# Kernel tuning notes

Hardware: AMD Instinct MI355X
Metric: run time of the kernel (lower is better)

## Reference

```python
import jax, jax.numpy as jnp
import numpy as np

B, L, D, P = 8, 2048, 1024, 256


def _ln(x):
    # LayerNorm without scale/offset (haiku default eps=1e-5)
    m = x.mean(-1, keepdims=True)
    v = x.var(-1, keepdims=True)
    return (x - m) * jax.lax.rsqrt(v + 1e-5)


def _s5(u, Lam_re, Lam_im, B_re, B_im, C_re, C_im, D_diag, log_step):
    # S5 diagonal SSM, ZOH discretization, parallel associative scan.
    Lam = Lam_re + 1j * Lam_im                      # (P,)
    dt = jnp.exp(log_step)                          # (P,)
    Lam_bar = jnp.exp(Lam * dt)                     # (P,)
    Bc = B_re + 1j * B_im                           # (P, D)
    B_bar = ((Lam_bar - 1.0) / Lam)[:, None] * Bc   # (P, D)
    Bu = jnp.einsum('bld,pd->blp', u.astype(B_bar.dtype), B_bar)  # (B, L, P)
    A = jnp.broadcast_to(Lam_bar, Bu.shape)

    def binop(e1, e2):
        a1, b1 = e1
        a2, b2 = e2
        return a1 * a2, a2 * b1 + b2

    _, xs = jax.lax.associative_scan(binop, (A, Bu), axis=1)  # (B, L, P)
    Cc = C_re + 1j * C_im                            # (D, P)
    return 2.0 * jnp.einsum('blp,dp->bld', xs, Cc).real + D_diag * u


def setup_inputs() -> dict:
    key = jax.random.key(0)
    ks = jax.random.split(key, 16)
    inp = {
        'y': jax.random.normal(ks[0], (B, L, D), jnp.float32),
        't': jax.random.normal(ks[1], (B, D), jnp.float32),
        # modulation projection m: Linear(D -> 6D)  (random instead of zero-init so output is non-trivial)
        'Wm': jax.random.normal(ks[2], (D, 6 * D), jnp.float32) * 0.02,
        'bm': jax.random.normal(ks[3], (6 * D,), jnp.float32) * 0.02,
        # S5Dual params
        'Lam_re': -0.5 * jnp.ones((P,), jnp.float32),
        'Lam_im': jnp.pi * jnp.arange(P, dtype=jnp.float32),
        'B_re': jax.random.normal(ks[4], (P, D), jnp.float32) / np.sqrt(D),
        'B_im': jax.random.normal(ks[5], (P, D), jnp.float32) / np.sqrt(D),
        'C_re': jax.random.normal(ks[6], (D, P), jnp.float32) / np.sqrt(P),
        'C_im': jax.random.normal(ks[7], (D, P), jnp.float32) / np.sqrt(P),
        'D_diag': jax.random.normal(ks[8], (D,), jnp.float32),
        'log_step': jax.random.uniform(ks[9], (P,), jnp.float32,
                                       np.log(0.001), np.log(0.1)),
        # AdaLN (norm2) projection: Linear(D -> 2D)
        'Wc': jax.random.normal(ks[10], (D, 2 * D), jnp.float32) * 0.02,
        'bc': jax.random.normal(ks[11], (2 * D,), jnp.float32) * 0.02,
        # FeedForward: pre Linear(D -> 4D), pos Linear(4D -> D) (random instead of zero-init)
        'W1': jax.random.normal(ks[12], (D, 4 * D), jnp.float32) / np.sqrt(D),
        'b1': jnp.zeros((4 * D,), jnp.float32),
        'W2': jax.random.normal(ks[13], (4 * D, D), jnp.float32) / np.sqrt(4 * D) * 0.1,
        'b2': jnp.zeros((D,), jnp.float32),
    }
    return inp


def reference(y, t, Wm, bm, Lam_re, Lam_im, B_re, B_im, C_re, C_im,
              D_diag, log_step, Wc, bc, W1, b1, W2, b2):
    # m(t) -> 6-way split
    mod = t @ Wm + bm
    shift_a, scale_a, gate_a, shift_ff, scale_ff, gate_ff = jnp.split(mod, 6, axis=-1)

    # S5 block with AdaLN-style modulation
    y_mod = _ln(y) * (1 + scale_a[:, None]) + shift_a[:, None]
    a_y = _s5(y_mod, Lam_re, Lam_im, B_re, B_im, C_re, C_im, D_diag, log_step)
    y = y + gate_a[:, None] * a_y

    # FFN block: norm2 is AdaLN(cond=t) composed with modulate(shift_ff, scale_ff)
    cond = t @ Wc + bc
    scale_c, shift_c = jnp.split(cond, 2, axis=-1)
    y_norm = _ln(y) * (1 + scale_c[:, None]) + shift_c[:, None]
    y_mod = y_norm * (1 + scale_ff[:, None]) + shift_ff[:, None]
    h = jax.nn.gelu(y_mod @ W1 + b1)
    ff_y = h @ W2 + b2
    return y + gate_ff[:, None] * ff_y
```

## Files before the change

### kernel.cpp

```cpp
#include <hip/hip_runtime.h>
#include <hip/hip_bf16.h>

#define Bsz 8
#define Lseq 2048
#define Dm 1024
#define Pst 256
#define BL (Bsz*Lseq)

typedef short bf16x8 __attribute__((ext_vector_type(8)));
typedef float f32x4  __attribute__((ext_vector_type(4)));

__device__ __forceinline__ float4 ldg4(const float* p){ return *reinterpret_cast<const float4*>(p); }
__device__ __forceinline__ ushort f2bf(float f){
    __hip_bfloat16 h = __float2bfloat16(f);
    return *reinterpret_cast<ushort*>(&h);
}
__device__ __forceinline__ float bf2f(ushort u){
    __hip_bfloat16 h = *reinterpret_cast<__hip_bfloat16*>(&u);
    return __bfloat162float(h);
}

__global__ __launch_bounds__(256) void proj_k(
    const float* __restrict__ T, const float* __restrict__ W,
    const float* __restrict__ bias, float* __restrict__ Out, int N)
{
    __shared__ float ts[Dm];
    int b = blockIdx.y;
    int j = blockIdx.x * 256 + threadIdx.x;
    for (int i = threadIdx.x; i < Dm; i += 256) ts[i] = T[b*Dm + i];
    __syncthreads();
    float s = bias[j];
    #pragma unroll 4
    for (int d = 0; d < Dm; ++d) s += ts[d] * W[(size_t)d*N + j];
    Out[(size_t)b*N + j] = s;
}

__global__ __launch_bounds__(256) void ssm_setup_k(
    const float* __restrict__ Lam_re, const float* __restrict__ Lam_im,
    const float* __restrict__ B_re, const float* __restrict__ B_im,
    const float* __restrict__ log_step, float* __restrict__ lam, ushort* __restrict__ Bbar_bf)
{
    int p = blockIdx.x;
    float lr = Lam_re[p], li = Lam_im[p];
    float dt = expf(log_step[p]);
    float e  = expf(lr*dt);
    float cr = e * cosf(li*dt);
    float ci = e * sinf(li*dt);
    float d2 = lr*lr + li*li;
    float nr = cr - 1.0f, ni = ci;
    float gr = (nr*lr + ni*li) / d2;
    float gi = (ni*lr - nr*li) / d2;
    if (threadIdx.x == 0) { lam[2*p] = cr; lam[2*p+1] = ci; }
    for (int d = threadIdx.x; d < Dm; d += 256) {
        float br = B_re[(size_t)p*Dm + d], bi = B_im[(size_t)p*Dm + d];
        Bbar_bf[(size_t)p*Dm + d]         = f2bf(gr*br - gi*bi);
        Bbar_bf[(size_t)(Pst+p)*Dm + d]   = f2bf(gr*bi + gi*br);
    }
}

__global__ __launch_bounds__(256) void ccat_k(
    const float* __restrict__ C_re, const float* __restrict__ C_im, ushort* __restrict__ Ccat_bf)
{
    int d = blockIdx.x;
    int p = threadIdx.x;
    Ccat_bf[(size_t)d*(2*Pst) + p]       = f2bf( 2.0f*C_re[(size_t)d*Pst + p]);
    Ccat_bf[(size_t)d*(2*Pst) + Pst + p] = f2bf(-2.0f*C_im[(size_t)d*Pst + p]);
}

__global__ __launch_bounds__(256) void transp_k(
    const float* __restrict__ in, ushort* __restrict__ out, int R, int C)
{
    __shared__ float tile[32][33];
    int tx = threadIdx.x & 31, ty = threadIdx.x >> 5;
    int r0 = blockIdx.y*32, c0 = blockIdx.x*32;
    #pragma unroll
    for (int j = 0; j < 4; ++j)
        tile[ty + j*8][tx] = in[(size_t)(r0 + ty + j*8)*C + c0 + tx];
    __syncthreads();
    #pragma unroll
    for (int j = 0; j < 4; ++j)
        out[(size_t)(c0 + ty + j*8)*R + r0 + tx] = f2bf(tile[tx][ty + j*8]);
}

template<int MODE>
__global__ __launch_bounds__(256) void ln_mod_k(
    const float* __restrict__ X, ushort* __restrict__ Y,
    const float* __restrict__ mod, const float* __restrict__ cond)
{
    int row = blockIdx.x;
    int b = row >> 11;
    int t = threadIdx.x;
    const float* xr = X + (size_t)row*Dm;
    float4 v = ldg4(xr + t*4);
    float s  = v.x + v.y + v.z + v.w;
    float ss = v.x*v.x + v.y*v.y + v.z*v.z + v.w*v.w;
    #pragma unroll
    for (int o = 32; o > 0; o >>= 1) { s += __shfl_down(s, o); ss += __shfl_down(ss, o); }
    __shared__ float red[8];
    int wid = t >> 6;
    if ((t & 63) == 0) { red[wid] = s; red[4+wid] = ss; }
    __syncthreads();
    float S  = red[0]+red[1]+red[2]+red[3];
    float SS = red[4]+red[5]+red[6]+red[7];
    float mean = S * (1.0f/Dm);
    float var  = SS * (1.0f/Dm) - mean*mean;
    float rstd = rsqrtf(var + 1e-5f);
    int d0 = t*4;
    float xv[4] = {v.x, v.y, v.z, v.w};
    ushort o4[4];
    #pragma unroll
    for (int q = 0; q < 4; ++q) {
        int d = d0 + q;
        float ln = (xv[q] - mean) * rstd;
        float r;
        if (MODE == 0) {
            r = ln * (1.0f + mod[(size_t)b*6144 + 1024 + d]) + mod[(size_t)b*6144 + d];
        } else {
            float yn = ln * (1.0f + cond[(size_t)b*2048 + d]) + cond[(size_t)b*2048 + 1024 + d];
            r = yn * (1.0f + mod[(size_t)b*6144 + 4096 + d]) + mod[(size_t)b*6144 + 3072 + d];
        }
        o4[q] = f2bf(r);
    }
    *reinterpret_cast<ushort4*>(Y + (size_t)row*Dm + d0) =
        make_ushort4(o4[0], o4[1], o4[2], o4[3]);
}

__global__ __launch_bounds__(256) void scan1_k(
    const float* __restrict__ Bu, const float* __restrict__ lam, float* __restrict__ carry)
{
    int bc = blockIdx.x;
    int b = bc >> 5, c = bc & 31;
    int p = threadIdx.x;
    float ar = lam[2*p], ai = lam[2*p+1];
    float xr = 0.f, xi = 0.f;
    const float* base = Bu + ((size_t)(b*Lseq + c*64))*(2*Pst);
    #pragma unroll 4
    for (int i = 0; i < 64; ++i) {
        float br = base[(size_t)i*(2*Pst) + p];
        float bi = base[(size_t)i*(2*Pst) + Pst + p];
        float nxr = ar*xr - ai*xi + br;
        float nxi = ar*xi + ai*xr + bi;
        xr = nxr; xi = nxi;
    }
    carry[((size_t)bc*Pst + p)*2]     = xr;
    carry[((size_t)bc*Pst + p)*2 + 1] = xi;
}

__global__ __launch_bounds__(256) void scan2_k(float* __restrict__ carry, const float* __restrict__ lam)
{
    int b = blockIdx.x;
    int p = threadIdx.x;
    float ar = lam[2*p], ai = lam[2*p+1];
    float pr = ar, pi = ai;
    #pragma unroll
    for (int s = 0; s < 6; ++s) { float nr = pr*pr - pi*pi, ni = 2.f*pr*pi; pr = nr; pi = ni; }
    float sr = 0.f, si = 0.f;
    for (int c = 0; c < 32; ++c) {
        size_t idx = ((size_t)(b*32 + c)*Pst + p)*2;
        float tr = carry[idx], ti = carry[idx+1];
        carry[idx] = sr; carry[idx+1] = si;
        float nr = pr*sr - pi*si + tr;
        float ni = pr*si + pi*sr + ti;
        sr = nr; si = ni;
    }
}

__global__ __launch_bounds__(256) void scan3_k(
    float* __restrict__ Bu, const float* __restrict__ lam, const float* __restrict__ carry)
{
    int bc = blockIdx.x;
    int b = bc >> 5, c = bc & 31;
    int p = threadIdx.x;
    float ar = lam[2*p], ai = lam[2*p+1];
    float xr = carry[((size_t)bc*Pst + p)*2];
    float xi = carry[((size_t)bc*Pst + p)*2 + 1];
    float* base = Bu + ((size_t)(b*Lseq + c*64))*(2*Pst);
    #pragma unroll 4
    for (int i = 0; i < 64; ++i) {
        float br = base[(size_t)i*(2*Pst) + p];
        float bi = base[(size_t)i*(2*Pst) + Pst + p];
        float nxr = ar*xr - ai*xi + br;
        float nxi = ar*xi + ai*xr + bi;
        xr = nxr; xi = nxi;
        base[(size_t)i*(2*Pst) + p] = xr;
        base[(size_t)i*(2*Pst) + Pst + p] = xi;
    }
}

#define BKP 72

template<int EPI, int AFP32>
__global__ __launch_bounds__(256) void gemm_mfma_k(
    const void* __restrict__ Av, const ushort* __restrict__ Bt, float* __restrict__ C,
    int M, int N, int K,
    const float* __restrict__ ep0, const float* __restrict__ ep1,
    const float* __restrict__ ep2, const ushort* __restrict__ ep3u, int m0)
{
    __shared__ ushort As[128*BKP];
    __shared__ ushort Bs[128*BKP];
    int tid = threadIdx.x;
    int bx = blockIdx.x, by = blockIdx.y;
    int w = tid >> 6, l = tid & 63;
    int wr = w >> 1, wc = w & 1;
    int lr = l & 15, lk = l >> 4;

    f32x4 acc[4][4];
    #pragma unroll
    for (int i = 0; i < 4; ++i)
        #pragma unroll
        for (int j = 0; j < 4; ++j)
            #pragma unroll
            for (int q = 0; q < 4; ++q) acc[i][j][q] = 0.f;

    const ushort* Ab = (const ushort*)Av;
    const float*  Af = (const float*)Av;

    for (int kt = 0; kt < K; kt += 64) {
        if (AFP32) {
            #pragma unroll
            for (int j = 0; j < 8; ++j) {
                int idx = tid + j*256;
                int r = idx >> 4, f4 = idx & 15;
                float4 v = ldg4(Af + (size_t)(by*128 + r)*K + kt + f4*4);
                *reinterpret_cast<ushort4*>(&As[r*BKP + f4*4]) =
                    make_ushort4(f2bf(v.x), f2bf(v.y), f2bf(v.z), f2bf(v.w));
            }
        } else {
            #pragma unroll
            for (int j = 0; j < 4; ++j) {
                int idx = tid + j*256;
                int r = idx >> 3, kc = idx & 7;
                int4 v = *reinterpret_cast<const int4*>(Ab + (size_t)(by*128 + r)*K + kt + kc*8);
                *reinterpret_cast<int4*>(&As[r*BKP + kc*8]) = v;
            }
        }
        #pragma unroll
        for (int j = 0; j < 4; ++j) {
            int idx = tid + j*256;
            int r = idx >> 3, kc = idx & 7;
            int4 v = *reinterpret_cast<const int4*>(Bt + (size_t)(bx*128 + r)*K + kt + kc*8);
            *reinterpret_cast<int4*>(&Bs[r*BKP + kc*8]) = v;
        }
        __syncthreads();
        #pragma unroll
        for (int mk = 0; mk < 2; ++mk) {
            bf16x8 a[4], b[4];
            #pragma unroll
            for (int mi = 0; mi < 4; ++mi)
                a[mi] = *reinterpret_cast<bf16x8*>(&As[(wr*64 + mi*16 + lr)*BKP + mk*32 + lk*8]);
            #pragma unroll
            for (int ni = 0; ni < 4; ++ni)
                b[ni] = *reinterpret_cast<bf16x8*>(&Bs[(wc*64 + ni*16 + lr)*BKP + mk*32 + lk*8]);
            #pragma unroll
            for (int mi = 0; mi < 4; ++mi)
                #pragma unroll
                for (int ni = 0; ni < 4; ++ni)
                    acc[mi][ni] = __builtin_amdgcn_mfma_f32_16x16x32_bf16(
                        a[mi], b[ni], acc[mi][ni], 0, 0, 0);
        }
        __syncthreads();
    }

    int row0 = by*128 + wr*64;
    int col0 = bx*128 + wc*64;
    #pragma unroll
    for (int mi = 0; mi < 4; ++mi) {
        #pragma unroll
        for (int ni = 0; ni < 4; ++ni) {
            int n = col0 + ni*16 + lr;
            #pragma unroll
            for (int q = 0; q < 4; ++q) {
                int m = row0 + mi*16 + lk*4 + q;
                float v = acc[mi][ni][q];
                if (EPI == 0) {
                    C[(size_t)m*N + n] = v;
                } else if (EPI == 1) {
                    int b = m >> 11;
                    float g  = ep1[(size_t)b*6144 + 2048 + n];
                    float dd = ep2[n];
                    float uu = bf2f(ep3u[(size_t)m*Dm + n]);
                    C[(size_t)m*Dm + n] = ep0[(size_t)m*Dm + n] + g*(v + dd*uu);
                } else if (EPI == 2) {
                    float x = v + ep0[n];
                    float x3 = x*x*x;
                    float r = 0.5f*x*(1.0f + tanhf(0.7978845608028654f*(x + 0.044715f*x3)));
                    ((ushort*)C)[(size_t)m*N + n] = f2bf(r);
                } else {
                    int gm = m0 + m; int b = gm >> 11;
                    float g = ep1[(size_t)b*6144 + 5120 + n];
                    C[(size_t)gm*Dm + n] += g*(v + ep0[n]);
                }
            }
        }
    }
}

extern "C" void kernel_launch(void* const* d_in, const int* in_sizes, int n_in,
                              void* d_out, int out_size, void* d_ws, size_t ws_size,
                              hipStream_t stream) {
    const float* y      = (const float*)d_in[0];
    const float* t      = (const float*)d_in[1];
    const float* Wm     = (const float*)d_in[2];
    const float* bm     = (const float*)d_in[3];
    const float* Lam_re = (const float*)d_in[4];
    const float* Lam_im = (const float*)d_in[5];
    const float* B_re   = (const float*)d_in[6];
    const float* B_im   = (const float*)d_in[7];
    const float* C_re   = (const float*)d_in[8];
    const float* C_im   = (const float*)d_in[9];
    const float* Ddiag  = (const float*)d_in[10];
    const float* lstep  = (const float*)d_in[11];
    const float* Wc     = (const float*)d_in[12];
    const float* bcn    = (const float*)d_in[13];
    const float* W1     = (const float*)d_in[14];
    const float* b1     = (const float*)d_in[15];
    const float* W2     = (const float*)d_in[16];
    const float* b2     = (const float*)d_in[17];
    float* out = (float*)d_out;
    char* ws = (char*)d_ws;

    ushort* u_bf    = (ushort*)ws;
    float*  Bu      = (float*)(ws + (32ull<<20));
    ushort* Bbar_bf = (ushort*)(ws + (64ull<<20));
    ushort* Ccat_bf = (ushort*)(ws + (65ull<<20));
    ushort* W1t     = (ushort*)(ws + (66ull<<20));
    ushort* W2t     = (ushort*)(ws + (74ull<<20));
    float*  mod     = (float*)(ws + (82ull<<20));
    float*  cond    = (float*)(ws + (82ull<<20) + 196608);
    float*  lam     = (float*)(ws + (82ull<<20) + 262144);
    float*  carry   = (float*)(ws + (82ull<<20) + 327680);
    ushort* y2_bf = u_bf;
    ushort* h_bf  = (ushort*)Bu;

    proj_k<<<dim3(24,8),256,0,stream>>>(t, Wm, bm, mod, 6144);
    proj_k<<<dim3(8,8),256,0,stream>>>(t, Wc, bcn, cond, 2048);
    ssm_setup_k<<<256,256,0,stream>>>(Lam_re, Lam_im, B_re, B_im, lstep, lam, Bbar_bf);
    ccat_k<<<1024,256,0,stream>>>(C_re, C_im, Ccat_bf);
    transp_k<<<dim3(128,32),256,0,stream>>>(W1, W1t, 1024, 4096);
    transp_k<<<dim3(32,128),256,0,stream>>>(W2, W2t, 4096, 1024);
    ln_mod_k<0><<<BL,256,0,stream>>>(y, u_bf, mod, nullptr);
    gemm_mfma_k<0,0><<<dim3(4,128),256,0,stream>>>(u_bf, Bbar_bf, Bu, BL, 512, 1024,
                                                   nullptr, nullptr, nullptr, nullptr, 0);
    scan1_k<<<256,256,0,stream>>>(Bu, lam, carry);
    scan2_k<<<8,256,0,stream>>>(carry, lam);
    scan3_k<<<256,256,0,stream>>>(Bu, lam, carry);
    gemm_mfma_k<1,1><<<dim3(8,128),256,0,stream>>>(Bu, Ccat_bf, out, BL, 1024, 512,
                                                   y, mod, Ddiag, u_bf, 0);
    ln_mod_k<1><<<BL,256,0,stream>>>(out, y2_bf, mod, cond);
    for (int mc = 0; mc < 4; ++mc) {
        const ushort* y2c = y2_bf + (size_t)mc*4096*Dm;
        gemm_mfma_k<2,0><<<dim3(32,32),256,0,stream>>>(y2c, W1t, (float*)h_bf, 4096, 4096, 1024,
                                                       b1, nullptr, nullptr, nullptr, 0);
        gemm_mfma_k<3,0><<<dim3(8,32),256,0,stream>>>(h_bf, W2t, out, 4096, 1024, 4096,
                                                      b2, mod, nullptr, nullptr, mc*4096);
    }
}
```

Measured before the change: 1.162 ms.

## Batch modulation projections across B with split-K atomics; swizzle GEMM workgroup order

The small t@W projections now compute all 8 batch rows per thread. Each W element is loaded once instead of once per batch, and the D dimension is split into 128-wide chunks that are reduced with atomicAdd into a buffer zeroed with a memset. Separately, the MFMA GEMM remaps its linear workgroup index with an XCD-style swizzle (stride by groups of 8) so that neighbouring tiles share cache. The atomics make the sums nondeterministic in order, and they add a memset launch.

```diff
diff --git a/kernel.cpp b/kernel.cpp
--- a/kernel.cpp
+++ b/kernel.cpp
@@ -20,19 +20,29 @@
     return __bfloat162float(h);
 }
 
-__global__ __launch_bounds__(256) void proj_k(
+__global__ __launch_bounds__(256) void proj2_k(
     const float* __restrict__ T, const float* __restrict__ W,
     const float* __restrict__ bias, float* __restrict__ Out, int N)
 {
-    __shared__ float ts[Dm];
-    int b = blockIdx.y;
-    int j = blockIdx.x * 256 + threadIdx.x;
-    for (int i = threadIdx.x; i < Dm; i += 256) ts[i] = T[b*Dm + i];
+    __shared__ float ts[8][128];
+    int j = blockIdx.x*256 + threadIdx.x;
+    int d0 = blockIdx.y*128;
+    for (int i = threadIdx.x; i < 8*128; i += 256) {
+        int b = i >> 7, d = i & 127;
+        ts[b][d] = T[(size_t)b*Dm + d0 + d];
+    }
     __syncthreads();
-    float s = bias[j];
+    float acc[8] = {};
     #pragma unroll 4
-    for (int d = 0; d < Dm; ++d) s += ts[d] * W[(size_t)d*N + j];
-    Out[(size_t)b*N + j] = s;
+    for (int d = 0; d < 128; ++d) {
+        float w = W[(size_t)(d0 + d)*N + j];
+        #pragma unroll
+        for (int b = 0; b < 8; ++b) acc[b] += ts[b][d]*w;
+    }
+    float bv = (blockIdx.y == 0) ? bias[j] : 0.f;
+    #pragma unroll
+    for (int b = 0; b < 8; ++b)
+        atomicAdd(&Out[(size_t)b*N + j], acc[b] + bv);
 }
 
 __global__ __launch_bounds__(256) void ssm_setup_k(
@@ -199,7 +209,12 @@
     __shared__ ushort As[128*BKP];
     __shared__ ushort Bs[128*BKP];
     int tid = threadIdx.x;
-    int bx = blockIdx.x, by = blockIdx.y;
+    int nwg = gridDim.x * gridDim.y;
+    int lin = blockIdx.y * gridDim.x + blockIdx.x;
+    int cpx = nwg >> 3;
+    int swz = (lin & 7) * cpx + (lin >> 3);
+    int bx = swz % gridDim.x, by = swz / gridDim.x;
+
     int w = tid >> 6, l = tid & 63;
     int wr = w >> 1, wc = w & 1;
     int lr = l & 15, lk = l >> 4;
@@ -332,8 +347,9 @@
     ushort* y2_bf = u_bf;
     ushort* h_bf  = (ushort*)Bu;
 
-    proj_k<<<dim3(24,8),256,0,stream>>>(t, Wm, bm, mod, 6144);
-    proj_k<<<dim3(8,8),256,0,stream>>>(t, Wc, bcn, cond, 2048);
+    hipMemsetAsync(mod, 0, 262144, stream);
+    proj2_k<<<dim3(24,8),256,0,stream>>>(t, Wm, bm, mod, 6144);
+    proj2_k<<<dim3(8,8),256,0,stream>>>(t, Wc, bcn, cond, 2048);
     ssm_setup_k<<<256,256,0,stream>>>(Lam_re, Lam_im, B_re, B_im, lstep, lam, Bbar_bf);
     ccat_k<<<1024,256,0,stream>>>(C_re, C_im, Ccat_bf);
     transp_k<<<dim3(128,32),256,0,stream>>>(W1, W1t, 1024, 4096);
```

New measurement: 958.9 us. 17.5% less time.
